# Optimization experiments

Measured on AMD Instinct MI355X. Metric: run time of the kernel, lower is better.

The kernel has to match this reference:

```python
import jax, jax.numpy as jnp
from jax import lax
import numpy as np

I, H = 16, 32  # input_size, hidden_size
B, T = 8192, 512


def setup_inputs() -> dict:
    key = jax.random.key(0)
    ks = jax.random.split(key, 8)
    s_ih = 1.0 / np.sqrt(H)
    x = jax.random.normal(ks[0], (B, T, I), dtype=jnp.float32)
    # PyTorch LSTM params, gate order i,f,g,o along the 4H dim
    W_ih = jax.random.uniform(ks[1], (4 * H, I), minval=-s_ih, maxval=s_ih, dtype=jnp.float32)
    W_hh = jax.random.uniform(ks[2], (4 * H, H), minval=-s_ih, maxval=s_ih, dtype=jnp.float32)
    b_ih = jax.random.uniform(ks[3], (4 * H,), minval=-s_ih, maxval=s_ih, dtype=jnp.float32)
    b_hh = jax.random.uniform(ks[4], (4 * H,), minval=-s_ih, maxval=s_ih, dtype=jnp.float32)
    W_fc = jax.random.uniform(ks[5], (1, H), minval=-s_ih, maxval=s_ih, dtype=jnp.float32)
    b_fc = jax.random.uniform(ks[6], (1,), minval=-s_ih, maxval=s_ih, dtype=jnp.float32)
    return {"x": x, "W_ih": W_ih, "W_hh": W_hh, "b_ih": b_ih, "b_hh": b_hh,
            "W_fc": W_fc, "b_fc": b_fc}


def reference(x, W_ih, W_hh, b_ih, b_hh, W_fc, b_fc):
    # Precompute input contribution for all timesteps: [B, T, 4H]
    xg = jnp.einsum('bti,gi->btg', x, W_ih) + b_ih + b_hh

    def step(carry, g_t):  # g_t: [B, 4H]
        h, c = carry
        gates = g_t + h @ W_hh.T
        i, f, g, o = jnp.split(gates, 4, axis=-1)
        c = jax.nn.sigmoid(f) * c + jax.nn.sigmoid(i) * jnp.tanh(g)
        h = jax.nn.sigmoid(o) * jnp.tanh(c)
        return (h, c), None

    h0 = jnp.zeros((x.shape[0], H), dtype=x.dtype)
    (h_last, _), _ = lax.scan(step, (h0, h0), jnp.swapaxes(xg, 0, 1))
    # last_hidden -> dropout (eval mode: identity) -> fc -> squeeze
    out = h_last @ W_fc.T + b_fc  # [B, 1]
    return out.squeeze(-1)  # [B]
```

## Files before the change

### kernel.cpp

```cpp
#include <hip/hip_runtime.h>


typedef float f4 __attribute__((ext_vector_type(4)));
typedef __bf16 bf8v __attribute__((ext_vector_type(8)));

constexpr int ISZ = 16, HSZ = 32, TT = 512, BB = 8192;
constexpr int HSTR = 72;
constexpr int XSTR = 40;
constexpr int GSTR = 34;

#define MFMA32(a, b, c) __builtin_amdgcn_mfma_f32_16x16x32_bf16((a), (b), (c), 0, 0, 0)

__device__ __forceinline__ float fsig(float x) {
  return __builtin_amdgcn_rcpf(1.0f + __builtin_amdgcn_exp2f(-1.44269504f * x));
}

__device__ __forceinline__ void split8(const float* v, bf8v& hi, bf8v& lo) {
#pragma unroll
  for (int i = 0; i < 8; ++i) {
    const __bf16 h = (__bf16)v[i];
    hi[i] = h;
    lo[i] = (__bf16)(v[i] - (float)h);
  }
}

__global__ __launch_bounds__(512, 4) void lstm_mfma(
    const float* __restrict__ x, const float* __restrict__ W_ih,
    const float* __restrict__ W_hh, const float* __restrict__ b_ih,
    const float* __restrict__ b_hh, const float* __restrict__ W_fc,
    const float* __restrict__ b_fc, float* __restrict__ out) {
  __shared__ __align__(16) __bf16 hl[2][16][HSTR];
  __shared__ __align__(16) __bf16 xs[2][16][XSTR];
  __shared__ __align__(16) float gbuf[4][16][GSTR];

  const int tid = threadIdx.x;
  const int wv = tid >> 6;
  const int g = wv & 3;
  const int uh = wv >> 2;
  const int L = tid & 63;
  const int m = L & 15;
  const int q = L >> 4;
  const int row0 = blockIdx.x * 16;
  const int uw = uh * 16 + m;
  const int j = g * 32 + uw;

  const int eR = wv * 2 + (L >> 5);
  const int eu = L & 31;

  bf8v bih1, bih2, bhh1, bhh2;
  f4 biasv;
  {
    float wh[8];
    *(f4*)&wh[0] = *(const f4*)(W_hh + j * HSZ + 8 * q);
    *(f4*)&wh[4] = *(const f4*)(W_hh + j * HSZ + 8 * q + 4);
    split8(wh, bhh1, bhh2);
    float wi[8];
    const int k8 = (q & 1) * 8;
    *(f4*)&wi[0] = *(const f4*)(W_ih + j * ISZ + k8);
    *(f4*)&wi[4] = *(const f4*)(W_ih + j * ISZ + k8 + 4);
    split8(wi, bih1, bih2);
    const float bb = b_ih[j] + b_hh[j];
    biasv = (f4){bb, bb, bb, bb};
  }

  for (int i = tid; i < 2 * 16 * HSTR; i += 512) ((__bf16*)hl)[i] = (__bf16)0.0f;
  const int xr = tid >> 4, xi = tid & 15;
  const float* xbase = x + (size_t)(row0 + xr) * TT * ISZ + xi;
  if (tid < 256) {
    const float v = xbase[0];
    const __bf16 h = (__bf16)v;
    xs[0][xr][xi] = h;
    xs[0][xr][16 + xi] = (__bf16)(v - (float)h);
  }
  __syncthreads();

  bf8v axn = *(const bf8v*)&xs[0][m][8 * q];
  f4 accx = MFMA32(axn, bih1, biasv);
  accx = MFMA32(axn, bih2, accx);
  float xnext = 0.0f;
  if (tid < 256) xnext = xbase[ISZ];

  float cst = 0.0f;

  for (int t = 0; t < TT; ++t) {
    const int p = t & 1;
    const bf8v ah1 = *(const bf8v*)&hl[p][m][8 * q];
    const bf8v ah2 = *(const bf8v*)&hl[p][m][32 + 8 * q];

    if (tid < 256) {
      const __bf16 xh = (__bf16)xnext;
      xs[p ^ 1][xr][xi] = xh;
      xs[p ^ 1][xr][16 + xi] = (__bf16)(xnext - (float)xh);
    }

    f4 a = MFMA32(ah1, bhh1, accx);
    a = MFMA32(ah2, bhh1, a);
    a = MFMA32(ah1, bhh2, a);

#pragma unroll
    for (int r = 0; r < 4; ++r) gbuf[g][q * 4 + r][uw] = a[r];
    __syncthreads();

    const int tl = (t + 2 < TT) ? t + 2 : TT - 1;
    if (tid < 256) xnext = xbase[(size_t)tl * ISZ];

    axn = *(const bf8v*)&xs[p ^ 1][m][8 * q];
    accx = MFMA32(axn, bih1, biasv);
    accx = MFMA32(axn, bih2, accx);

    const float vi = gbuf[0][eR][eu];
    const float vf = gbuf[1][eR][eu];
    const float vg = gbuf[2][eR][eu];
    const float vo = gbuf[3][eR][eu];

    const float ig = fsig(vi);
    const float fg = fsig(vf);
    const float gv = 2.0f * fsig(2.0f * vg) - 1.0f;
    const float og = fsig(vo);
    const float cc = fg * cst + ig * gv;
    cst = cc;
    const float th = 2.0f * fsig(2.0f * cc) - 1.0f;
    const float h = og * th;
    const __bf16 h1 = (__bf16)h;
    hl[p ^ 1][eR][eu] = h1;
    hl[p ^ 1][eR][32 + eu] = (__bf16)(h - (float)h1);
    __syncthreads();
  }

  if (tid < 16) {
    float s = b_fc[0];
#pragma unroll 8
    for (int uu = 0; uu < HSZ; ++uu) {
      const float h = (float)hl[0][tid][uu] + (float)hl[0][tid][32 + uu];
      s += h * W_fc[uu];
    }
    out[row0 + tid] = s;
  }
}

extern "C" void kernel_launch(void* const* d_in, const int* in_sizes, int n_in,
                              void* d_out, int out_size, void* d_ws, size_t ws_size,
                              hipStream_t stream) {
  const float* x    = (const float*)d_in[0];
  const float* W_ih = (const float*)d_in[1];
  const float* W_hh = (const float*)d_in[2];
  const float* b_ih = (const float*)d_in[3];
  const float* b_hh = (const float*)d_in[4];
  const float* W_fc = (const float*)d_in[5];
  const float* b_fc = (const float*)d_in[6];
  float* out = (float*)d_out;

  dim3 grid(BB / 16);
  dim3 block(512);
  lstm_mfma<<<grid, block, 0, stream>>>(x, W_ih, W_hh, b_ih, b_hh, W_fc, b_fc, out);
}
```

Before: 638.5 us.

## Split block into consumer and producer waves for input-gate precompute

Doubles the block to 1024 threads. Eight new producer waves compute the input projection W_ih·x + bias one step ahead and stage x loads, writing the results into a double-buffered shared gx array. The original eight waves now only do the recurrent MFMAs and the gate nonlinearities. The aim is to take the input-projection work and global x loads off the recurrent critical path, at the cost of larger blocks, more shared memory and more threads taking part in each barrier.

Result: slower. 707.1 us (+10.7%).

```diff
diff --git a/kernel.cpp b/kernel.cpp
--- a/kernel.cpp
+++ b/kernel.cpp
@@ -24,7 +24,7 @@
   }
 }
 
-__global__ __launch_bounds__(512, 4) void lstm_mfma(
+__global__ __launch_bounds__(1024, 8) void lstm_mfma(
     const float* __restrict__ x, const float* __restrict__ W_ih,
     const float* __restrict__ W_hh, const float* __restrict__ b_ih,
     const float* __restrict__ b_hh, const float* __restrict__ W_fc,
@@ -32,98 +32,118 @@
   __shared__ __align__(16) __bf16 hl[2][16][HSTR];
   __shared__ __align__(16) __bf16 xs[2][16][XSTR];
   __shared__ __align__(16) float gbuf[4][16][GSTR];
+  __shared__ __align__(16) float gx[2][4][16][GSTR];
 
   const int tid = threadIdx.x;
   const int wv = tid >> 6;
-  const int g = wv & 3;
-  const int uh = wv >> 2;
+  const bool isProd = wv >= 8;
+  const int gw = wv & 3;
+  const int uh = (wv >> 2) & 1;
   const int L = tid & 63;
   const int m = L & 15;
   const int q = L >> 4;
   const int row0 = blockIdx.x * 16;
   const int uw = uh * 16 + m;
-  const int j = g * 32 + uw;
+  const int j = gw * 32 + uw;
 
-  const int eR = wv * 2 + (L >> 5);
+  const int eR = (wv & 7) * 2 + (L >> 5);
   const int eu = L & 31;
 
-  bf8v bih1, bih2, bhh1, bhh2;
-  f4 biasv;
-  {
+  const bool doStage = (wv >= 8) && (wv < 12);
+  const int st = tid & 255;
+  const int xr = st >> 4, xi = st & 15;
+  const float* xbase = x + (size_t)(row0 + xr) * TT * ISZ + xi;
+
+  bf8v wA1, wA2;
+  f4 biasv = (f4){0.0f, 0.0f, 0.0f, 0.0f};
+  if (!isProd) {
     float wh[8];
     *(f4*)&wh[0] = *(const f4*)(W_hh + j * HSZ + 8 * q);
     *(f4*)&wh[4] = *(const f4*)(W_hh + j * HSZ + 8 * q + 4);
-    split8(wh, bhh1, bhh2);
+    split8(wh, wA1, wA2);
+  } else {
     float wi[8];
     const int k8 = (q & 1) * 8;
     *(f4*)&wi[0] = *(const f4*)(W_ih + j * ISZ + k8);
     *(f4*)&wi[4] = *(const f4*)(W_ih + j * ISZ + k8 + 4);
-    split8(wi, bih1, bih2);
+    split8(wi, wA1, wA2);
     const float bb = b_ih[j] + b_hh[j];
     biasv = (f4){bb, bb, bb, bb};
   }
 
-  for (int i = tid; i < 2 * 16 * HSTR; i += 512) ((__bf16*)hl)[i] = (__bf16)0.0f;
-  const int xr = tid >> 4, xi = tid & 15;
-  const float* xbase = x + (size_t)(row0 + xr) * TT * ISZ + xi;
-  if (tid < 256) {
-    const float v = xbase[0];
-    const __bf16 h = (__bf16)v;
-    xs[0][xr][xi] = h;
-    xs[0][xr][16 + xi] = (__bf16)(v - (float)h);
+  for (int i = tid; i < 2 * 16 * HSTR; i += 1024) ((__bf16*)hl)[i] = (__bf16)0.0f;
+  if (doStage) {
+    const float v0 = xbase[0];
+    const __bf16 h0 = (__bf16)v0;
+    xs[0][xr][xi] = h0;
+    xs[0][xr][16 + xi] = (__bf16)(v0 - (float)h0);
+    const float v1 = xbase[ISZ];
+    const __bf16 h1 = (__bf16)v1;
+    xs[1][xr][xi] = h1;
+    xs[1][xr][16 + xi] = (__bf16)(v1 - (float)h1);
+  }
+  __syncthreads();
+  if (isProd) {
+    const bf8v ax = *(const bf8v*)&xs[0][m][8 * q];
+    f4 a = MFMA32(ax, wA1, biasv);
+    a = MFMA32(ax, wA2, a);
+#pragma unroll
+    for (int r = 0; r < 4; ++r) gx[0][gw][q * 4 + r][uw] = a[r];
   }
   __syncthreads();
 
-  bf8v axn = *(const bf8v*)&xs[0][m][8 * q];
-  f4 accx = MFMA32(axn, bih1, biasv);
-  accx = MFMA32(axn, bih2, accx);
+  float cst = 0.0f;
   float xnext = 0.0f;
-  if (tid < 256) xnext = xbase[ISZ];
-
-  float cst = 0.0f;
+  f4 pacc;
 
   for (int t = 0; t < TT; ++t) {
     const int p = t & 1;
-    const bf8v ah1 = *(const bf8v*)&hl[p][m][8 * q];
-    const bf8v ah2 = *(const bf8v*)&hl[p][m][32 + 8 * q];
-
-    if (tid < 256) {
-      const __bf16 xh = (__bf16)xnext;
-      xs[p ^ 1][xr][xi] = xh;
-      xs[p ^ 1][xr][16 + xi] = (__bf16)(xnext - (float)xh);
+    if (!isProd) {
+      f4 c;
+#pragma unroll
+      for (int r = 0; r < 4; ++r) c[r] = gx[p][gw][q * 4 + r][uw];
+      const bf8v ah1 = *(const bf8v*)&hl[p][m][8 * q];
+      const bf8v ah2 = *(const bf8v*)&hl[p][m][32 + 8 * q];
+      f4 a = MFMA32(ah1, wA1, c);
+      a = MFMA32(ah2, wA1, a);
+      a = MFMA32(ah1, wA2, a);
+#pragma unroll
+      for (int r = 0; r < 4; ++r) gbuf[gw][q * 4 + r][uw] = a[r];
+    } else {
+      const bf8v ax = *(const bf8v*)&xs[p ^ 1][m][8 * q];
+      pacc = MFMA32(ax, wA1, biasv);
+      pacc = MFMA32(ax, wA2, pacc);
+      if (doStage) {
+        const int tl = (t + 2 < TT) ? t + 2 : TT - 1;
+        xnext = xbase[(size_t)tl * ISZ];
+      }
     }
-
-    f4 a = MFMA32(ah1, bhh1, accx);
-    a = MFMA32(ah2, bhh1, a);
-    a = MFMA32(ah1, bhh2, a);
-
+    __syncthreads();
+    if (!isProd) {
+      const float vi = gbuf[0][eR][eu];
+      const float vf = gbuf[1][eR][eu];
+      const float vg = gbuf[2][eR][eu];
+      const float vo = gbuf[3][eR][eu];
+      const float ig = fsig(vi);
+      const float fg = fsig(vf);
+      const float gv = 2.0f * fsig(2.0f * vg) - 1.0f;
+      const float og = fsig(vo);
+      const float cc = fg * cst + ig * gv;
+      cst = cc;
+      const float th = 2.0f * fsig(2.0f * cc) - 1.0f;
+      const float h = og * th;
+      const __bf16 h1 = (__bf16)h;
+      hl[p ^ 1][eR][eu] = h1;
+      hl[p ^ 1][eR][32 + eu] = (__bf16)(h - (float)h1);
+    } else {
 #pragma unroll
-    for (int r = 0; r < 4; ++r) gbuf[g][q * 4 + r][uw] = a[r];
-    __syncthreads();
-
-    const int tl = (t + 2 < TT) ? t + 2 : TT - 1;
-    if (tid < 256) xnext = xbase[(size_t)tl * ISZ];
-
-    axn = *(const bf8v*)&xs[p ^ 1][m][8 * q];
-    accx = MFMA32(axn, bih1, biasv);
-    accx = MFMA32(axn, bih2, accx);
-
-    const float vi = gbuf[0][eR][eu];
-    const float vf = gbuf[1][eR][eu];
-    const float vg = gbuf[2][eR][eu];
-    const float vo = gbuf[3][eR][eu];
-
-    const float ig = fsig(vi);
-    const float fg = fsig(vf);
-    const float gv = 2.0f * fsig(2.0f * vg) - 1.0f;
-    const float og = fsig(vo);
-    const float cc = fg * cst + ig * gv;
-    cst = cc;
-    const float th = 2.0f * fsig(2.0f * cc) - 1.0f;
-    const float h = og * th;
-    const __bf16 h1 = (__bf16)h;
-    hl[p ^ 1][eR][eu] = h1;
-    hl[p ^ 1][eR][32 + eu] = (__bf16)(h - (float)h1);
+      for (int r = 0; r < 4; ++r) gx[p ^ 1][gw][q * 4 + r][uw] = pacc[r];
+      if (doStage) {
+        const __bf16 xh = (__bf16)xnext;
+        xs[p][xr][xi] = xh;
+        xs[p][xr][16 + xi] = (__bf16)(xnext - (float)xh);
+      }
+    }
     __syncthreads();
   }
 
@@ -151,6 +171,6 @@
   float* out = (float*)d_out;
 
   dim3 grid(BB / 16);
-  dim3 block(512);
+  dim3 block(1024);
   lstm_mfma<<<grid, block, 0, stream>>>(x, W_ih, W_hh, b_ih, b_hh, W_fc, b_fc, out);
 }
```
